# Kernel optimization log

Hardware: AMD Instinct MI355X
Metric: run time of the kernel (lower is better)

The kernel has to match this reference:

```python
import jax, jax.numpy as jnp
import numpy as np

NUM_HEADS = 8
BLOCK_SIZE = 32   # tokens per block
WINDOW = 64       # window radius in blocks -> attends to blocks [i-64, i+64]


def setup_inputs() -> dict:
    key = jax.random.key(0)
    ks = jax.random.split(key, 5)
    B, N, C = 8, 8192, 512
    s = 0.02
    return {
        "x": jax.random.normal(ks[0], (B, N, C), dtype=jnp.float32),
        # torch Linear(dim, 3*dim): y = x @ W.T + b; we store W already transposed [in, out]
        "W_qkv": jax.random.normal(ks[1], (C, 3 * C), dtype=jnp.float32) * s,
        "b_qkv": jax.random.normal(ks[2], (3 * C,), dtype=jnp.float32) * s,
        "W_proj": jax.random.normal(ks[3], (C, C), dtype=jnp.float32) * s,
        "b_proj": jax.random.normal(ks[4], (C,), dtype=jnp.float32) * s,
    }


def reference(x, W_qkv, b_qkv, W_proj, b_proj):
    B, N, C = x.shape
    h = NUM_HEADS
    dh = C // h
    scale = jnp.asarray(dh, x.dtype) ** -0.5

    # qkv projection, then the module's head-interleaved split:
    # rearrange 'b n (h d) -> b h n d' with d = 3C/h, chunk(3) on last dim,
    # rearrange back 'b h n d -> b n (h d)'. Equivalent to:
    qkv = (x @ W_qkv + b_qkv).reshape(B, N, h, 3 * dh)
    q = qkv[..., :dh].reshape(B, N, C)
    k = qkv[..., dh:2 * dh].reshape(B, N, C)
    v = qkv[..., 2 * dh:].reshape(B, N, C)

    # dynamic blocking (N chosen divisible by BLOCK_SIZE -> no padding)
    nb = N // BLOCK_SIZE
    qb = q.reshape(B, nb, BLOCK_SIZE, C)
    kb = k.reshape(B, nb, BLOCK_SIZE, C)
    vb = v.reshape(B, nb, BLOCK_SIZE, C)

    # per-offset block attention: query block i, position s attends to
    # position s of every block j in [i-WINDOW, i+WINDOW]
    attn = jnp.einsum('bisc,bjsc->bisj', qb, kb) * scale  # [B, nb, s, nb]
    i_idx = jnp.arange(nb)[:, None]
    j_idx = jnp.arange(nb)[None, :]
    band = (j_idx >= i_idx - WINDOW) & (j_idx <= i_idx + WINDOW)  # [nb, nb]
    neg = jnp.finfo(attn.dtype).min
    attn = jnp.where(band[None, :, None, :], attn, neg)
    attn = jax.nn.softmax(attn, axis=-1)
    out = jnp.einsum('bisj,bjsc->bisc', attn, vb)  # [B, nb, s, C]
    out = out.reshape(B, N, C)

    # 'b n (h d) -> b n h d -> b n (h d)' is the identity
    return out @ W_proj + b_proj
```

## Files before the change

kernel.cpp:

```cpp
#include <hip/hip_runtime.h>
#include <hip/hip_bf16.h>
#include <stdint.h>

#define B_   8
#define N_   8192
#define C_   512
#define NB   256
#define WIN  64

typedef __attribute__((ext_vector_type(8))) short short8;
typedef __attribute__((ext_vector_type(4))) float f32x4;
typedef __hip_bfloat16 bf16;

__device__ __forceinline__ void gload_lds16(const void* g, void* l) {
  __builtin_amdgcn_global_load_lds((const __attribute__((address_space(1))) void*)g,
                                   (__attribute__((address_space(3))) void*)l, 16, 0, 0);
}

__device__ __forceinline__ f32x4 mfma16(short8 a, short8 b, f32x4 c) {
  return __builtin_amdgcn_mfma_f32_16x16x32_bf16(a, b, c, 0, 0, 0);
}


__global__ __launch_bounds__(256) void k_conv_x(const float4* __restrict__ x,
                                                ushort4* __restrict__ xb) {
  size_t idx = (size_t)blockIdx.x * 256 + threadIdx.x;
  float4 v = x[idx];
  union { ushort4 u; bf16 b[4]; } o;
  o.b[0] = __float2bfloat16(v.x); o.b[1] = __float2bfloat16(v.y);
  o.b[2] = __float2bfloat16(v.z); o.b[3] = __float2bfloat16(v.w);
  xb[idx] = o.u;
}

__global__ __launch_bounds__(256) void k_conv_wqkv(const float* __restrict__ W,
                                                   const float* __restrict__ bq,
                                                   bf16* __restrict__ Wt,
                                                   float* __restrict__ bperm) {
  int o = blockIdx.x;
  int part = o >> 9;
  int c = o & 511;
  int h = c >> 6, d = c & 63;
  int src = h * 192 + part * 64 + d;
  for (int kk = threadIdx.x; kk < 512; kk += 256)
    Wt[(size_t)o * 512 + kk] = __float2bfloat16(W[(size_t)kk * 1536 + src]);
  if (threadIdx.x == 0) bperm[o] = bq[src];
}

__global__ __launch_bounds__(256) void k_conv_wproj(const float* __restrict__ W,
                                                    bf16* __restrict__ Wt) {
  int o = blockIdx.x;
  for (int kk = threadIdx.x; kk < 512; kk += 256)
    Wt[(size_t)o * 512 + kk] = __float2bfloat16(W[(size_t)kk * 512 + o]);
}

template <int EPI>
__global__ __launch_bounds__(512, 2) void k_gemm(const bf16* __restrict__ A,
                                                 const bf16* __restrict__ Bt,
                                                 const float* __restrict__ bias,
                                                 bf16* __restrict__ qb,
                                                 bf16* __restrict__ kb,
                                                 bf16* __restrict__ vb,
                                                 float* __restrict__ outf,
                                                 int NT) {
  extern __shared__ bf16 sm[];
  const int tid = threadIdx.x;
  const int lane = tid & 63, wid = tid >> 6;
  const int wr = wid >> 2, wcn = wid & 3;
  const int l15 = lane & 15, l4 = lane >> 4;

  const int nwg = gridDim.x;
  const int cpx = nwg >> 3;
  const int swz = (blockIdx.x & 7) * cpx + (blockIdx.x >> 3);
  const int mt = swz / NT, nt = swz % NT;
  const size_t m0 = (size_t)mt * 256;
  const int n0 = nt * 256;

  f32x4 acc[8][4];
#pragma unroll
  for (int fi = 0; fi < 8; ++fi)
#pragma unroll
    for (int fj = 0; fj < 4; ++fj) acc[fi][fj] = (f32x4){0.f, 0.f, 0.f, 0.f};

#define STAGEG(slot, k0)                                                       \
  {                                                                            \
    bf16* Adst = sm + (slot) * 32768;                                          \
    bf16* Bdst = Adst + 16384;                                                 \
    _Pragma("unroll") for (int i = 0; i < 4; ++i) {                            \
      int li = i * 512 + tid;                                                  \
      int row = li >> 3, ch = li & 7;                                          \
      int chs = ch ^ (row & 7);                                                \
      gload_lds16(A + (m0 + row) * 512 + (k0) + chs * 8,                       \
                  (char*)Adst + li * 16);                                      \
      gload_lds16(Bt + (size_t)(n0 + row) * 512 + (k0) + chs * 8,              \
                  (char*)Bdst + li * 16);                                      \
    }                                                                          \
  }

  STAGEG(0, 0);
  for (int t = 0; t < 8; ++t) {
    if (t < 7) {
      STAGEG((t + 1) & 1, (t + 1) * 64);
      asm volatile("s_waitcnt vmcnt(8)" ::: "memory");
    } else {
      asm volatile("s_waitcnt vmcnt(0)" ::: "memory");
    }
    __builtin_amdgcn_s_barrier();
    __builtin_amdgcn_sched_barrier(0);
    const bf16* Ap = sm + (t & 1) * 32768;
    const bf16* Bp = Ap + 16384;
#pragma unroll
    for (int ks = 0; ks < 2; ++ks) {
      short8 a[8], b[4];
#pragma unroll
      for (int fi = 0; fi < 8; ++fi) {
        int ra = wr * 128 + fi * 16 + l15;
        a[fi] = *(const short8*)&Ap[ra * 64 + (((ks * 4 + l4) ^ (ra & 7)) << 3)];
      }
#pragma unroll
      for (int fj = 0; fj < 4; ++fj) {
        int rb = wcn * 64 + fj * 16 + l15;
        b[fj] = *(const short8*)&Bp[rb * 64 + (((ks * 4 + l4) ^ (rb & 7)) << 3)];
      }
      __builtin_amdgcn_s_setprio(1);
#pragma unroll
      for (int fi = 0; fi < 8; ++fi)
#pragma unroll
        for (int fj = 0; fj < 4; ++fj)
          acc[fi][fj] = mfma16(a[fi], b[fj], acc[fi][fj]);
      __builtin_amdgcn_s_setprio(0);
    }
    __builtin_amdgcn_sched_barrier(0);
    __builtin_amdgcn_s_barrier();
  }
#undef STAGEG

  if (EPI == 0) {
#pragma unroll
    for (int fi = 0; fi < 8; ++fi)
#pragma unroll
      for (int fj = 0; fj < 4; ++fj) {
        int o = n0 + wcn * 64 + fj * 16 + l15;
        float bia = bias[o];
        int part = o >> 9;
        int c = o & 511;
        bf16* dst = part == 0 ? qb : (part == 1 ? kb : vb);
#pragma unroll
        for (int r = 0; r < 4; ++r) {
          size_t m = m0 + wr * 128 + fi * 16 + l4 * 4 + r;
          int bidx = (int)(m >> 13);
          int n = (int)(m & 8191);
          int blk = n >> 5, s = n & 31;
          size_t di = (((size_t)(bidx * 32 + s) * 256 + blk) << 9) | c;
          dst[di] = __float2bfloat16(acc[fi][fj][r] + bia);
        }
      }
  } else {
#pragma unroll
    for (int fi = 0; fi < 8; ++fi)
#pragma unroll
      for (int fj = 0; fj < 4; ++fj) {
        int o = n0 + wcn * 64 + fj * 16 + l15;
        float bia = bias[o];
#pragma unroll
        for (int r = 0; r < 4; ++r) {
          size_t m = m0 + wr * 128 + fi * 16 + l4 * 4 + r;
          outf[m * 512 + o] = acc[fi][fj][r] + bia;
        }
      }
  }
}

__global__ __launch_bounds__(256) void k_transpose_v(const bf16* __restrict__ v,
                                                     bf16* __restrict__ vT) {
  __shared__ bf16 t[32][36];
  int bs = blockIdx.x, j0 = blockIdx.y * 32, c0 = blockIdx.z * 32;
  const bf16* src = v + (size_t)bs * NB * C_;
  bf16* dst = vT + (size_t)bs * C_ * NB;
  int r = threadIdx.x >> 3, c4 = (threadIdx.x & 7) * 4;
  *(ushort4*)&t[r][c4] = *(const ushort4*)(src + (size_t)(j0 + r) * C_ + c0 + c4);
  __syncthreads();
  union { ushort4 u; bf16 b[4]; } o;
  o.b[0] = t[c4 + 0][r]; o.b[1] = t[c4 + 1][r];
  o.b[2] = t[c4 + 2][r]; o.b[3] = t[c4 + 3][r];
  *(ushort4*)(dst + (size_t)(c0 + r) * NB + j0 + c4) = o.u;
}

__global__ __launch_bounds__(512) void k_attn(const bf16* __restrict__ qg,
                                              const bf16* __restrict__ kg,
                                              const bf16* __restrict__ vTg,
                                              bf16* __restrict__ outb) {
  __shared__ bf16 Qs[32][520];
  __shared__ float Ss[32][164];
  __shared__ bf16 Ps[32][168];
  __shared__ float rowsum[32];
  const int tid = threadIdx.x, lane = tid & 63, wid = tid >> 6;
  const int l15 = lane & 15, l4 = lane >> 4;
  const int gt = (blockIdx.x & 7) * 256 + (blockIdx.x >> 3);
  const int bs = gt >> 3;
  const int b = bs >> 5, s = bs & 31;
  const int i0 = (gt & 7) * 32;
  const int jlo = max(0, i0 - WIN);
  const int jhi = min(NB - 1, i0 + 31 + WIN);
  const int L = jhi - jlo + 1;
  const int nch16 = (L + 15) >> 4, L16 = nch16 << 4;
  const int nch32 = (L16 + 31) >> 5, L32 = nch32 << 5;
  const bf16* Qb = qg + (size_t)bs * NB * C_;
  const bf16* Kb = kg + (size_t)bs * NB * C_;
  const bf16* Vb = vTg + (size_t)bs * C_ * NB;

#pragma unroll
  for (int qq = 0; qq < 4; ++qq) {
    int li = qq * 512 + tid;
    int row = li >> 6, ch = li & 63;
    *(float4*)&Qs[row][ch * 8] = *(const float4*)(Qb + (size_t)(i0 + row) * C_ + ch * 8);
  }
  __syncthreads();

  for (int e = wid; e < 2 * nch16; e += 8) {
    int jc = e >> 1, qh = e & 1;
    f32x4 acc = (f32x4){0.f, 0.f, 0.f, 0.f};
    int jg = jlo + jc * 16 + l15;
    int jcl = min(jg, NB - 1);
    const bf16* kp = Kb + (size_t)jcl * C_ + l4 * 8;
    const bf16* q0 = &Qs[qh * 16 + l15][l4 * 8];
#pragma unroll
    for (int cc = 0; cc < 16; ++cc) {
      short8 bfr = *(const short8*)(kp + cc * 32);
      short8 a0 = *(const short8*)(q0 + cc * 32);
      acc = mfma16(a0, bfr, acc);
    }
#pragma unroll
    for (int r = 0; r < 4; ++r)
      Ss[qh * 16 + l4 * 4 + r][jc * 16 + l15] = acc[r] * 0.125f;
  }
  __syncthreads();

  {
    int row = tid >> 4, u = tid & 15;
    int i = i0 + row;
    int vlo = max(i - WIN, 0), vhi = min(i + WIN, NB - 1);
    float m = -1e30f;
    for (int jj = u; jj < L16; jj += 16) {
      int jg = jlo + jj;
      if (jg >= vlo && jg <= vhi) m = fmaxf(m, Ss[row][jj]);
    }
    m = fmaxf(m, __shfl_xor(m, 1));
    m = fmaxf(m, __shfl_xor(m, 2));
    m = fmaxf(m, __shfl_xor(m, 4));
    m = fmaxf(m, __shfl_xor(m, 8));
    float sum = 0.f;
    for (int jj = u; jj < L32; jj += 16) {
      float p = 0.f;
      int jg = jlo + jj;
      if (jj < L16 && jg >= vlo && jg <= vhi) p = __expf(Ss[row][jj] - m);
      sum += p;
      Ps[row][jj] = __float2bfloat16(p);
    }
    sum += __shfl_xor(sum, 1);
    sum += __shfl_xor(sum, 2);
    sum += __shfl_xor(sum, 4);
    sum += __shfl_xor(sum, 8);
    if (u == 0) rowsum[row] = sum;
  }
  __syncthreads();

  {
    const int c0 = wid * 64;
#pragma unroll
    for (int ic = 0; ic < 2; ++ic) {
#pragma unroll
      for (int f = 0; f < 4; ++f) {
        f32x4 acc = (f32x4){0.f, 0.f, 0.f, 0.f};
        int c = c0 + f * 16 + l15;
        const bf16* pr = &Ps[ic * 16 + l15][l4 * 8];
        for (int j32 = 0; j32 < nch32; ++j32) {
          int jg = jlo + j32 * 32 + l4 * 8;
          int jcl = (jg <= NB - 8) ? jg : 0;
          short8 a = *(const short8*)(pr + j32 * 32);
          short8 bfr = *(const short8*)(Vb + (size_t)c * NB + jcl);
          acc = mfma16(a, bfr, acc);
        }
#pragma unroll
        for (int r = 0; r < 4; ++r) {
          int il = ic * 16 + l4 * 4 + r;
          float val = acc[r] / rowsum[il];
          int n = (i0 + il) * 32 + s;
          outb[((size_t)b * N_ + n) * C_ + c] = __float2bfloat16(val);
        }
      }
    }
  }
}

extern "C" void kernel_launch(void* const* d_in, const int* in_sizes, int n_in,
                              void* d_out, int out_size, void* d_ws, size_t ws_size,
                              hipStream_t stream) {
  const float* x = (const float*)d_in[0];
  const float* Wqkv = (const float*)d_in[1];
  const float* bqkv = (const float*)d_in[2];
  const float* Wproj = (const float*)d_in[3];
  const float* bproj = (const float*)d_in[4];

  char* ws = (char*)d_ws;
  const size_t SLOT = 67108864ull;
  bf16* slotA = (bf16*)ws;
  bf16* slotB = (bf16*)(ws + SLOT);
  bf16* Wqkv_t = (bf16*)(ws + 2 * SLOT);
  bf16* Wproj_t = (bf16*)(ws + 2 * SLOT + 1572864);
  float* bias_perm = (float*)(ws + 2 * SLOT + 1572864 + 524288);
  bf16* qbuf = (bf16*)d_out;
  bf16* kbuf = qbuf + 33554432ull;

  static int attr_done = 0;
  if (!attr_done) {
    hipFuncSetAttribute((const void*)k_gemm<0>,
                        hipFuncAttributeMaxDynamicSharedMemorySize, 131072);
    hipFuncSetAttribute((const void*)k_gemm<1>,
                        hipFuncAttributeMaxDynamicSharedMemorySize, 131072);
    attr_done = 1;
  }

  k_conv_x<<<32768, 256, 0, stream>>>((const float4*)x, (ushort4*)slotA);
  k_conv_wqkv<<<1536, 256, 0, stream>>>(Wqkv, bqkv, Wqkv_t, bias_perm);
  k_conv_wproj<<<512, 256, 0, stream>>>(Wproj, Wproj_t);

  k_gemm<0><<<256 * 6, 512, 131072, stream>>>(slotA, Wqkv_t, bias_perm,
                                              qbuf, kbuf, slotB, nullptr, 6);
  k_transpose_v<<<dim3(256, 8, 16), 256, 0, stream>>>(slotB, slotA);
  k_attn<<<2048, 512, 0, stream>>>(qbuf, kbuf, slotA, slotB);
  k_gemm<1><<<256 * 2, 512, 131072, stream>>>(slotB, Wproj_t, bproj,
                                              nullptr, nullptr, nullptr, (float*)d_out, 2);
}
```

Measured before the change: 400.8 us.

## Rewrite banded attention as flash-style online softmax with LDS-staged K/V double buffering

The attention kernel now walks the key band in 32-block chunks with an online softmax (running max, sum and rescale factor) instead of materialising the whole score row. Q, K and V tiles are staged into XOR-swizzled LDS with direct global-to-LDS loads, and the next K tile is prefetched while the current chunk is computed. The QK product is split across waves along the reduction dimension and combined through LDS. This is meant to cut uncoalesced global V reads and latency stalls, at the cost of about 139 KB of LDS per block (one block per CU) and more barriers per chunk.

```diff
diff --git a/kernel.cpp b/kernel.cpp
--- a/kernel.cpp
+++ b/kernel.cpp
@@ -185,14 +185,29 @@
   *(ushort4*)(dst + (size_t)(c0 + r) * NB + j0 + c4) = o.u;
 }
 
+#define QS_OFF   0
+#define KB_OFF   32768
+#define VB_OFF   98304
+#define SS_OFF   131072
+#define PS_OFF   135296
+#define SR_OFF   137856
+#define MR_OFF   141952
+#define LR_OFF   142080
+#define AL_OFF   142208
+#define ATTN_LDS 142336
+
 __global__ __launch_bounds__(512) void k_attn(const bf16* __restrict__ qg,
                                               const bf16* __restrict__ kg,
                                               const bf16* __restrict__ vTg,
                                               bf16* __restrict__ outb) {
-  __shared__ bf16 Qs[32][520];
-  __shared__ float Ss[32][164];
-  __shared__ bf16 Ps[32][168];
-  __shared__ float rowsum[32];
+  extern __shared__ char smc[];
+  float* Ssf  = (float*)(smc + SS_OFF);
+  bf16*  Psb  = (bf16*)(smc + PS_OFF);
+  float* Sred = (float*)(smc + SR_OFF);
+  float* mrow = (float*)(smc + MR_OFF);
+  float* lrow = (float*)(smc + LR_OFF);
+  float* alph = (float*)(smc + AL_OFF);
+
   const int tid = threadIdx.x, lane = tid & 63, wid = tid >> 6;
   const int l15 = lane & 15, l4 = lane >> 4;
   const int gt = (blockIdx.x & 7) * 256 + (blockIdx.x >> 3);
@@ -201,92 +216,161 @@
   const int i0 = (gt & 7) * 32;
   const int jlo = max(0, i0 - WIN);
   const int jhi = min(NB - 1, i0 + 31 + WIN);
-  const int L = jhi - jlo + 1;
-  const int nch16 = (L + 15) >> 4, L16 = nch16 << 4;
-  const int nch32 = (L16 + 31) >> 5, L32 = nch32 << 5;
+  const int nch = (jhi - jlo + 1) >> 5;
   const bf16* Qb = qg + (size_t)bs * NB * C_;
   const bf16* Kb = kg + (size_t)bs * NB * C_;
   const bf16* Vb = vTg + (size_t)bs * C_ * NB;
 
-#pragma unroll
-  for (int qq = 0; qq < 4; ++qq) {
-    int li = qq * 512 + tid;
-    int row = li >> 6, ch = li & 63;
-    *(float4*)&Qs[row][ch * 8] = *(const float4*)(Qb + (size_t)(i0 + row) * C_ + ch * 8);
-  }
-  __syncthreads();
-
-  for (int e = wid; e < 2 * nch16; e += 8) {
-    int jc = e >> 1, qh = e & 1;
-    f32x4 acc = (f32x4){0.f, 0.f, 0.f, 0.f};
-    int jg = jlo + jc * 16 + l15;
-    int jcl = min(jg, NB - 1);
-    const bf16* kp = Kb + (size_t)jcl * C_ + l4 * 8;
-    const bf16* q0 = &Qs[qh * 16 + l15][l4 * 8];
-#pragma unroll
-    for (int cc = 0; cc < 16; ++cc) {
-      short8 bfr = *(const short8*)(kp + cc * 32);
-      short8 a0 = *(const short8*)(q0 + cc * 32);
-      acc = mfma16(a0, bfr, acc);
-    }
-#pragma unroll
-    for (int r = 0; r < 4; ++r)
-      Ss[qh * 16 + l4 * 4 + r][jc * 16 + l15] = acc[r] * 0.125f;
-  }
-  __syncthreads();
-
+  const int qh_qk = (wid >> 2) & 1, jh = (wid >> 1) & 1, ks = wid & 1;
+  const int qh_pv = wid >> 2, cq = wid & 3;
+
+  f32x4 O[8];
+#pragma unroll
+  for (int f = 0; f < 8; ++f) O[f] = (f32x4){0.f, 0.f, 0.f, 0.f};
+
+  if (tid < 32) { mrow[tid] = -1e30f; lrow[tid] = 0.f; }
+
+#pragma unroll
+  for (int q = 0; q < 4; ++q) {
+    int li = q * 512 + tid;
+    int row = li >> 6, g = (li & 63) ^ (row & 15);
+    gload_lds16(Qb + (size_t)(i0 + row) * C_ + g * 8, smc + QS_OFF + li * 16);
+  }
+#pragma unroll
+  for (int q = 0; q < 4; ++q) {
+    int li = q * 512 + tid;
+    int row = li >> 6, g = (li & 63) ^ (row & 15);
+    gload_lds16(Kb + (size_t)(jlo + row) * C_ + g * 8, smc + KB_OFF + li * 16);
+  }
+
+  for (int t = 0; t < nch; ++t) {
+    const int j0 = jlo + t * 32;
+    asm volatile("s_waitcnt vmcnt(0) lgkmcnt(0)" ::: "memory");
+    __builtin_amdgcn_s_barrier();
+    __builtin_amdgcn_sched_barrier(0);
+
+#pragma unroll
+    for (int q = 0; q < 4; ++q) {
+      int li = q * 512 + tid;
+      int c = li >> 2, g = (li & 3) ^ (c & 3);
+      gload_lds16(Vb + (size_t)c * NB + j0 + g * 8, smc + VB_OFF + li * 16);
+    }
+    if (t + 1 < nch) {
+      int jn = j0 + 32;
+      char* kdst = smc + KB_OFF + ((t + 1) & 1) * 32768;
+#pragma unroll
+      for (int q = 0; q < 4; ++q) {
+        int li = q * 512 + tid;
+        int row = li >> 6, g = (li & 63) ^ (row & 15);
+        gload_lds16(Kb + (size_t)(jn + row) * C_ + g * 8, kdst + li * 16);
+      }
+    }
+
+    {
+      const int arow = qh_qk * 16 + l15;
+      const int brow = jh * 16 + l15;
+      const char* Qbase = smc + QS_OFF + arow * 1024;
+      const char* Kbase = smc + KB_OFF + (t & 1) * 32768 + brow * 1024;
+      f32x4 a0 = (f32x4){0.f, 0.f, 0.f, 0.f}, a1 = a0;
+      __builtin_amdgcn_s_setprio(1);
+#pragma unroll
+      for (int cc = 0; cc < 8; ++cc) {
+        int sa = (ks * 32 + cc * 4 + l4) ^ (arow & 15);
+        int sb = (ks * 32 + cc * 4 + l4) ^ (brow & 15);
+        short8 av = *(const short8*)(Qbase + sa * 16);
+        short8 bv = *(const short8*)(Kbase + sb * 16);
+        if (cc & 1) a1 = mfma16(av, bv, a1);
+        else        a0 = mfma16(av, bv, a0);
+      }
+      __builtin_amdgcn_s_setprio(0);
+      f32x4 acc = a0 + a1;
+      if (ks) {
+        *(f32x4*)&Sred[(wid >> 1) * 256 + lane * 4] = acc;
+      }
+      asm volatile("s_waitcnt lgkmcnt(0)" ::: "memory");
+      __builtin_amdgcn_s_barrier();
+      __builtin_amdgcn_sched_barrier(0);
+      if (!ks) {
+        f32x4 su = acc + *(f32x4*)&Sred[(wid >> 1) * 256 + lane * 4];
+        int jg = j0 + jh * 16 + l15;
+#pragma unroll
+        for (int r = 0; r < 4; ++r) {
+          int i_in = qh_qk * 16 + l4 * 4 + r;
+          int i_abs = i0 + i_in;
+          bool valid = (jg >= i_abs - WIN) && (jg <= i_abs + WIN);
+          Ssf[i_in * 33 + jh * 16 + l15] = valid ? su[r] * 0.125f : -1e30f;
+        }
+      }
+      asm volatile("s_waitcnt lgkmcnt(0)" ::: "memory");
+      __builtin_amdgcn_s_barrier();
+      __builtin_amdgcn_sched_barrier(0);
+    }
+
+    {
+      int row = tid >> 4, u = tid & 15;
+      float s0 = Ssf[row * 33 + u], s1 = Ssf[row * 33 + u + 16];
+      float mc = fmaxf(s0, s1);
+      mc = fmaxf(mc, __shfl_xor(mc, 1));
+      mc = fmaxf(mc, __shfl_xor(mc, 2));
+      mc = fmaxf(mc, __shfl_xor(mc, 4));
+      mc = fmaxf(mc, __shfl_xor(mc, 8));
+      float mo = mrow[row];
+      float mn = fmaxf(mo, mc);
+      float a = __expf(mo - mn);
+      float p0 = __expf(s0 - mn), p1 = __expf(s1 - mn);
+      float ps = p0 + p1;
+      ps += __shfl_xor(ps, 1);
+      ps += __shfl_xor(ps, 2);
+      ps += __shfl_xor(ps, 4);
+      ps += __shfl_xor(ps, 8);
+      if (u == 0) {
+        lrow[row] = lrow[row] * a + ps;
+        mrow[row] = mn;
+        alph[row] = a;
+      }
+      Psb[row * 40 + u] = __float2bfloat16(p0);
+      Psb[row * 40 + u + 16] = __float2bfloat16(p1);
+    }
+    if (t + 1 < nch)
+      asm volatile("s_waitcnt vmcnt(4) lgkmcnt(0)" ::: "memory");
+    else
+      asm volatile("s_waitcnt vmcnt(0) lgkmcnt(0)" ::: "memory");
+    __builtin_amdgcn_s_barrier();
+    __builtin_amdgcn_sched_barrier(0);
+
+    {
+      float ar[4];
+#pragma unroll
+      for (int r = 0; r < 4; ++r) ar[r] = alph[qh_pv * 16 + l4 * 4 + r];
+      short8 pa = *(const short8*)(smc + PS_OFF + (qh_pv * 16 + l15) * 80 + l4 * 16);
+      __builtin_amdgcn_s_setprio(1);
+#pragma unroll
+      for (int f = 0; f < 8; ++f) {
+        int c = cq * 128 + f * 16 + l15;
+        short8 vv = *(const short8*)(smc + VB_OFF + c * 64 + ((l4 ^ (c & 3)) << 4));
+#pragma unroll
+        for (int r = 0; r < 4; ++r) O[f][r] *= ar[r];
+        O[f] = mfma16(pa, vv, O[f]);
+      }
+      __builtin_amdgcn_s_setprio(0);
+    }
+    __builtin_amdgcn_sched_barrier(0);
+  }
+
+  asm volatile("s_waitcnt lgkmcnt(0)" ::: "memory");
+  __builtin_amdgcn_s_barrier();
   {
-    int row = tid >> 4, u = tid & 15;
-    int i = i0 + row;
-    int vlo = max(i - WIN, 0), vhi = min(i + WIN, NB - 1);
-    float m = -1e30f;
-    for (int jj = u; jj < L16; jj += 16) {
-      int jg = jlo + jj;
-      if (jg >= vlo && jg <= vhi) m = fmaxf(m, Ss[row][jj]);
-    }
-    m = fmaxf(m, __shfl_xor(m, 1));
-    m = fmaxf(m, __shfl_xor(m, 2));
-    m = fmaxf(m, __shfl_xor(m, 4));
-    m = fmaxf(m, __shfl_xor(m, 8));
-    float sum = 0.f;
-    for (int jj = u; jj < L32; jj += 16) {
-      float p = 0.f;
-      int jg = jlo + jj;
-      if (jj < L16 && jg >= vlo && jg <= vhi) p = __expf(Ss[row][jj] - m);
-      sum += p;
-      Ps[row][jj] = __float2bfloat16(p);
-    }
-    sum += __shfl_xor(sum, 1);
-    sum += __shfl_xor(sum, 2);
-    sum += __shfl_xor(sum, 4);
-    sum += __shfl_xor(sum, 8);
-    if (u == 0) rowsum[row] = sum;
-  }
-  __syncthreads();
-
-  {
-    const int c0 = wid * 64;
-#pragma unroll
-    for (int ic = 0; ic < 2; ++ic) {
-#pragma unroll
-      for (int f = 0; f < 4; ++f) {
-        f32x4 acc = (f32x4){0.f, 0.f, 0.f, 0.f};
-        int c = c0 + f * 16 + l15;
-        const bf16* pr = &Ps[ic * 16 + l15][l4 * 8];
-        for (int j32 = 0; j32 < nch32; ++j32) {
-          int jg = jlo + j32 * 32 + l4 * 8;
-          int jcl = (jg <= NB - 8) ? jg : 0;
-          short8 a = *(const short8*)(pr + j32 * 32);
-          short8 bfr = *(const short8*)(Vb + (size_t)c * NB + jcl);
-          acc = mfma16(a, bfr, acc);
-        }
-#pragma unroll
-        for (int r = 0; r < 4; ++r) {
-          int il = ic * 16 + l4 * 4 + r;
-          float val = acc[r] / rowsum[il];
-          int n = (i0 + il) * 32 + s;
-          outb[((size_t)b * N_ + n) * C_ + c] = __float2bfloat16(val);
-        }
+    float lr[4];
+#pragma unroll
+    for (int r = 0; r < 4; ++r) lr[r] = 1.f / lrow[qh_pv * 16 + l4 * 4 + r];
+#pragma unroll
+    for (int f = 0; f < 8; ++f) {
+      int c = cq * 128 + f * 16 + l15;
+#pragma unroll
+      for (int r = 0; r < 4; ++r) {
+        int il = qh_pv * 16 + l4 * 4 + r;
+        int n = (i0 + il) * 32 + s;
+        outb[((size_t)b * N_ + n) * C_ + c] = __float2bfloat16(O[f][r] * lr[r]);
       }
     }
   }
@@ -317,6 +401,8 @@
                         hipFuncAttributeMaxDynamicSharedMemorySize, 131072);
     hipFuncSetAttribute((const void*)k_gemm<1>,
                         hipFuncAttributeMaxDynamicSharedMemorySize, 131072);
+    hipFuncSetAttribute((const void*)k_attn,
+                        hipFuncAttributeMaxDynamicSharedMemorySize, ATTN_LDS);
     attr_done = 1;
   }
 
@@ -327,7 +413,7 @@
   k_gemm<0><<<256 * 6, 512, 131072, stream>>>(slotA, Wqkv_t, bias_perm,
                                               qbuf, kbuf, slotB, nullptr, 6);
   k_transpose_v<<<dim3(256, 8, 16), 256, 0, stream>>>(slotB, slotA);
-  k_attn<<<2048, 512, 0, stream>>>(qbuf, kbuf, slotA, slotB);
+  k_attn<<<2048, 512, ATTN_LDS, stream>>>(qbuf, kbuf, slotA, slotB);
   k_gemm<1><<<256 * 2, 512, 131072, stream>>>(slotB, Wproj_t, bproj,
                                               nullptr, nullptr, nullptr, (float*)d_out, 2);
 }
```

New measurement: 339.1 us. 1.18x faster.
